# Kernel optimization log

Measured on AMD Instinct MI355X. Metric: run time of the kernel, lower is better.

## Reference

```python
import jax, jax.numpy as jnp
import numpy as np

NUM_K = 10
T = 1.0  # softmax temperature (forward default)


def setup_inputs() -> dict:
    key = jax.random.key(0)
    k1, k2, k3, k4 = jax.random.split(key, 4)
    B, H, P, D = 64, 12, 197, 64
    return {
        "att_s": jax.random.normal(k1, (B, H, P, P), dtype=jnp.float32),
        "att_t": jax.random.normal(k2, (B, H, P, P), dtype=jnp.float32),
        "v_s": jax.random.normal(k3, (B, H, P, D), dtype=jnp.float32),
        "v_t": jax.random.normal(k4, (B, H, P, D), dtype=jnp.float32),
    }


def _topk_masked_attend(att, v):
    # att: [B,H,P,P] logits, v: [B,H,P,D]
    a = jax.nn.softmax(att / T, axis=-1)
    # kth-largest value per row acts as the threshold (torch.topk semantics)
    margin = jax.lax.top_k(a, NUM_K)[0][..., -1]           # [B,H,P]
    a = a * (a >= margin[..., None])                        # keep top-k entries
    norm = a.sum(-1)                                        # [B,H,P]
    return jnp.einsum("bhpq,bhqd->bhpd", a, v) / norm[..., None]


def reference(att_s, att_t, v_s, v_t):
    out_s = _topk_masked_attend(att_s, v_s)
    out_t = _topk_masked_attend(att_t, v_t)
    # nn.MSELoss default reduction='mean'
    return jnp.mean(jnp.square(out_s - out_t))
```

## Files before the change

kernel.cpp:

```cpp
#include <hip/hip_runtime.h>
#include <cstdint>
#include <cfloat>

#define NK 10
constexpr int Pp   = 197;
constexpr int Dd   = 64;
constexpr int ROWS = 64 * 12 * 197;
constexpr int BLK  = 256;
constexpr int RPB  = 256;
constexpr int NBLK = ROWS / RPB;
constexpr int CH   = 32;
constexpr int NFULL = Pp / CH;
constexpr int TAIL  = Pp - NFULL * CH;
constexpr float INV_N = 1.0f / 9682944.0f;

__device__ __forceinline__ uint32_t fbits(float x) { return __float_as_uint(x); }
__device__ __forceinline__ float    bfl(uint32_t u) { return __uint_as_float(u); }

template <int CW>
__device__ __forceinline__ void consume_chunk(const float (*tile)[CH + 1], int t,
                                              float a[NK]) {
#pragma unroll
  for (int j = 0; j < CW; ++j) {
    float x = tile[t][j];
#pragma unroll
    for (int s = 0; s < NK - 1; ++s) a[s] = fmaxf(a[s], fminf(x, a[s + 1]));
    a[NK - 1] = fmaxf(a[NK - 1], x);
  }
}

__device__ __forceinline__ void select_rows(const float* __restrict__ A,
                                            float (*tile)[CH + 1],
                                            float (*wpk)[NK], int t,
                                            int blockRow0) {
  float a[NK];
#pragma unroll
  for (int k = 0; k < NK; ++k) a[k] = -FLT_MAX;

  const float* slab = A + (size_t)blockRow0 * Pp;

  for (int c = 0; c < NFULL; ++c) {
    __syncthreads();
    const float* cbase = slab + c * CH;
#pragma unroll 8
    for (int e = t; e < RPB * CH; e += BLK) {
      int r = e >> 5, j = e & 31;
      float x = cbase[r * Pp + j];
      uint32_t u = (fbits(x) & 0xFFFFFF00u) | (uint32_t)(c * CH + j);
      tile[r][j] = bfl(u);
    }
    __syncthreads();
    consume_chunk<CH>(tile, t, a);
  }
  __syncthreads();
  {
    const float* cbase = slab + NFULL * CH;
    for (int e = t; e < RPB * TAIL; e += BLK) {
      int r = e / TAIL, j = e % TAIL;
      float x = cbase[r * Pp + j];
      uint32_t u = (fbits(x) & 0xFFFFFF00u) | (uint32_t)(NFULL * CH + j);
      tile[r][j] = bfl(u);
    }
  }
  __syncthreads();
  consume_chunk<TAIL>(tile, t, a);

  float mx = a[NK - 1];
  float e[NK], s = 0.f;
#pragma unroll
  for (int k = 0; k < NK; ++k) {
    e[k] = __expf(a[k] - mx);
    s += e[k];
  }
  float inv = 1.0f / s;
#pragma unroll
  for (int k = 0; k < NK; ++k) {
    float w = e[k] * inv;
    uint32_t wb = (fbits(w) & 0xFFFFFF00u) | (fbits(a[k]) & 0xFFu);
    wpk[t][k] = bfl(wb);
  }
}

__global__ __launch_bounds__(BLK) void topk_mse_kernel(
    const float* __restrict__ att_s, const float* __restrict__ att_t,
    const float* __restrict__ v_s, const float* __restrict__ v_t,
    float* __restrict__ out) {
  __shared__ float tile[RPB][CH + 1];
  __shared__ float wpk[2][RPB][NK];
  __shared__ float red[BLK / 64];

  const int t = threadIdx.x;
  const int blockRow0 = blockIdx.x * RPB;

  select_rows(att_s, tile, wpk[0], t, blockRow0);
  select_rows(att_t, tile, wpk[1], t, blockRow0);
  __syncthreads();

  const int wv = t >> 6, l = t & 63;
  float accsum = 0.f;
  for (int i = 0; i < 64; ++i) {
    int rl = (wv << 6) | i;
    int rg = blockRow0 + rl;
    int bh = rg / Pp;
    const float* vsb = v_s + (size_t)bh * (Pp * Dd);
    const float* vtb = v_t + (size_t)bh * (Pp * Dd);
    float acc = 0.f;
#pragma unroll
    for (int k = 0; k < NK; ++k) {
      float w = wpk[0][rl][k];
      int idx = (int)(fbits(w) & 0xFFu);
      acc = fmaf(w, vsb[idx * Dd + l], acc);
    }
#pragma unroll
    for (int k = 0; k < NK; ++k) {
      float w = wpk[1][rl][k];
      int idx = (int)(fbits(w) & 0xFFu);
      acc = fmaf(-w, vtb[idx * Dd + l], acc);
    }
    accsum = fmaf(acc, acc, accsum);
  }

#pragma unroll
  for (int off = 32; off > 0; off >>= 1) accsum += __shfl_xor(accsum, off, 64);
  if (l == 0) red[wv] = accsum;
  __syncthreads();
  if (t == 0) {
    float tot = (red[0] + red[1]) + (red[2] + red[3]);
    atomicAdd(out, tot * INV_N);
  }
}

extern "C" void kernel_launch(void* const* d_in, const int* in_sizes, int n_in,
                              void* d_out, int out_size, void* d_ws,
                              size_t ws_size, hipStream_t stream) {
  const float* att_s = (const float*)d_in[0];
  const float* att_t = (const float*)d_in[1];
  const float* v_s = (const float*)d_in[2];
  const float* v_t = (const float*)d_in[3];
  float* out = (float*)d_out;

  hipMemsetAsync(out, 0, sizeof(float), stream);
  topk_mse_kernel<<<NBLK, BLK, 0, stream>>>(att_s, att_t, v_s, v_t, out);
}
```

Measured before the change: 427.0 us.

## Prefetch next attention chunk into registers and broadcast top-k weights via wave shuffles

```diff
diff --git a/kernel.cpp b/kernel.cpp
--- a/kernel.cpp
+++ b/kernel.cpp
@@ -18,52 +18,78 @@
 __device__ __forceinline__ float    bfl(uint32_t u) { return __uint_as_float(u); }
 
 template <int CW>
-__device__ __forceinline__ void consume_chunk(const float (*tile)[CH + 1], int t,
+__device__ __forceinline__ void consume_chunk(const float* __restrict__ trow,
                                               float a[NK]) {
 #pragma unroll
   for (int j = 0; j < CW; ++j) {
-    float x = tile[t][j];
+    float x = trow[j];
 #pragma unroll
     for (int s = 0; s < NK - 1; ++s) a[s] = fmaxf(a[s], fminf(x, a[s + 1]));
     a[NK - 1] = fmaxf(a[NK - 1], x);
   }
 }
 
+__device__ __forceinline__ void load_chunk_regs(const float* __restrict__ slab,
+                                                int c, int t, float pf[CH]) {
+  if (c < NFULL) {
+    const int r0 = t >> 5, j = t & 31;
+    const uint32_t col = (uint32_t)(c * CH + j);
+    const float* p = slab + c * CH + r0 * Pp + j;
+#pragma unroll
+    for (int i = 0; i < CH; ++i) {
+      float x = p[i * 8 * Pp];
+      pf[i] = bfl((fbits(x) & 0xFFFFFF00u) | col);
+    }
+  } else {
+    const float* cbase = slab + NFULL * CH;
+#pragma unroll
+    for (int i = 0; i < TAIL; ++i) {
+      int e = t + i * BLK;
+      int r = e / TAIL, j = e % TAIL;
+      float x = cbase[r * Pp + j];
+      pf[i] = bfl((fbits(x) & 0xFFFFFF00u) | (uint32_t)(NFULL * CH + j));
+    }
+  }
+}
+
+__device__ __forceinline__ void store_chunk(float (*tile)[CH + 1], int c, int t,
+                                            const float pf[CH]) {
+  if (c < NFULL) {
+    const int r0 = t >> 5, j = t & 31;
+#pragma unroll
+    for (int i = 0; i < CH; ++i) tile[r0 + 8 * i][j] = pf[i];
+  } else {
+#pragma unroll
+    for (int i = 0; i < TAIL; ++i) {
+      int e = t + i * BLK;
+      tile[e / TAIL][e % TAIL] = pf[i];
+    }
+  }
+}
+
 __device__ __forceinline__ void select_rows(const float* __restrict__ A,
                                             float (*tile)[CH + 1],
-                                            float (*wpk)[NK], int t,
+                                            float wsel[NK], int t,
                                             int blockRow0) {
   float a[NK];
 #pragma unroll
   for (int k = 0; k < NK; ++k) a[k] = -FLT_MAX;
 
   const float* slab = A + (size_t)blockRow0 * Pp;
+  float pf[CH];
 
-  for (int c = 0; c < NFULL; ++c) {
+  load_chunk_regs(slab, 0, t, pf);
+  for (int c = 0; c <= NFULL; ++c) {
     __syncthreads();
-    const float* cbase = slab + c * CH;
-#pragma unroll 8
-    for (int e = t; e < RPB * CH; e += BLK) {
-      int r = e >> 5, j = e & 31;
-      float x = cbase[r * Pp + j];
-      uint32_t u = (fbits(x) & 0xFFFFFF00u) | (uint32_t)(c * CH + j);
-      tile[r][j] = bfl(u);
-    }
+    store_chunk(tile, c, t, pf);
     __syncthreads();
-    consume_chunk<CH>(tile, t, a);
-  }
-  __syncthreads();
-  {
-    const float* cbase = slab + NFULL * CH;
-    for (int e = t; e < RPB * TAIL; e += BLK) {
-      int r = e / TAIL, j = e % TAIL;
-      float x = cbase[r * Pp + j];
-      uint32_t u = (fbits(x) & 0xFFFFFF00u) | (uint32_t)(NFULL * CH + j);
-      tile[r][j] = bfl(u);
+    if (c < NFULL) {
+      load_chunk_regs(slab, c + 1, t, pf);
+      consume_chunk<CH>(tile[t], a);
+    } else {
+      consume_chunk<TAIL>(tile[t], a);
     }
   }
-  __syncthreads();
-  consume_chunk<TAIL>(tile, t, a);
 
   float mx = a[NK - 1];
   float e[NK], s = 0.f;
@@ -76,25 +102,23 @@
 #pragma unroll
   for (int k = 0; k < NK; ++k) {
     float w = e[k] * inv;
-    uint32_t wb = (fbits(w) & 0xFFFFFF00u) | (fbits(a[k]) & 0xFFu);
-    wpk[t][k] = bfl(wb);
+    wsel[k] = bfl((fbits(w) & 0xFFFFFF00u) | (fbits(a[k]) & 0xFFu));
   }
 }
 
-__global__ __launch_bounds__(BLK) void topk_mse_kernel(
+__global__ __launch_bounds__(BLK, 4) void topk_mse_kernel(
     const float* __restrict__ att_s, const float* __restrict__ att_t,
     const float* __restrict__ v_s, const float* __restrict__ v_t,
     float* __restrict__ out) {
   __shared__ float tile[RPB][CH + 1];
-  __shared__ float wpk[2][RPB][NK];
   __shared__ float red[BLK / 64];
 
   const int t = threadIdx.x;
   const int blockRow0 = blockIdx.x * RPB;
 
-  select_rows(att_s, tile, wpk[0], t, blockRow0);
-  select_rows(att_t, tile, wpk[1], t, blockRow0);
-  __syncthreads();
+  float wsel[2][NK];
+  select_rows(att_s, tile, wsel[0], t, blockRow0);
+  select_rows(att_t, tile, wsel[1], t, blockRow0);
 
   const int wv = t >> 6, l = t & 63;
   float accsum = 0.f;
@@ -102,20 +126,20 @@
     int rl = (wv << 6) | i;
     int rg = blockRow0 + rl;
     int bh = rg / Pp;
-    const float* vsb = v_s + (size_t)bh * (Pp * Dd);
-    const float* vtb = v_t + (size_t)bh * (Pp * Dd);
+    const float* vsb = v_s + (size_t)bh * (Pp * Dd) + l;
+    const float* vtb = v_t + (size_t)bh * (Pp * Dd) + l;
     float acc = 0.f;
 #pragma unroll
     for (int k = 0; k < NK; ++k) {
-      float w = wpk[0][rl][k];
+      float w = __shfl(wsel[0][k], i, 64);
       int idx = (int)(fbits(w) & 0xFFu);
-      acc = fmaf(w, vsb[idx * Dd + l], acc);
+      acc = fmaf(w, vsb[idx * Dd], acc);
     }
 #pragma unroll
     for (int k = 0; k < NK; ++k) {
-      float w = wpk[1][rl][k];
+      float w = __shfl(wsel[1][k], i, 64);
       int idx = (int)(fbits(w) & 0xFFu);
-      acc = fmaf(-w, vtb[idx * Dd + l], acc);
+      acc = fmaf(-w, vtb[idx * Dd], acc);
     }
     accsum = fmaf(acc, acc, accsum);
   }
```

New measurement: 385.6 us. 1.11x faster.
